# Performance work log

Hardware: AMD Instinct MI355X
Metric: run time of the kernel (lower is better)

## Reference

```python
import jax, jax.numpy as jnp
import numpy as np
from jax import lax

NH = 8          # heads
DK = 64         # total key/query depth
DV = 64         # total value depth
DKH = DK // NH  # per-head key depth = 8
DVH = DV // NH  # per-head value depth = 8
H = W = 32
CIN = 256
FILTERS = 256


def rel_to_abs(x):
    # x: [B, N, L, 2L-1] relative logits -> [B, N, L, L] absolute logits
    B, N, L, _ = x.shape
    x = jnp.pad(x, ((0, 0), (0, 0), (0, 0), (0, 1)))          # [B,N,L,2L]
    flat = x.reshape(B, N, L * 2 * L)
    flat = jnp.pad(flat, ((0, 0), (0, 0), (0, L - 1)))        # [B,N,2L^2+L-1]
    final = flat.reshape(B, N, L + 1, 2 * L - 1)
    return final[:, :, :L, L - 1:]


def rel_logits_1d(q, rel_k, h, w, perm):
    # q: [B, NH, h, w, DKH], rel_k: [2w-1, DKH]
    B = q.shape[0]
    rel = jnp.einsum('bnxyd,md->bnxym', q, rel_k)             # [B,NH,h,w,2w-1]
    rel = rel.reshape(B, NH * h, w, 2 * w - 1)
    rel = rel_to_abs(rel)                                     # [B,NH*h,w,w]
    rel = rel.reshape(B, NH, h, w, w)[:, :, :, None]          # [B,NH,h,1,w,w]
    rel = jnp.broadcast_to(rel, (B, NH, h, h, w, w))          # tile over other axis
    rel = jnp.transpose(rel, perm)
    return rel.reshape(B, NH, h * w, h * w)


def setup_inputs() -> dict:
    key = jax.random.key(0)
    ks = jax.random.split(key, 6)
    s = lambda fan_in: 1.0 / np.sqrt(fan_in)
    return {
        'x': jax.random.normal(ks[0], (8, H, W, CIN), jnp.float32),
        'conv_w': jax.random.normal(ks[1], (3, 3, CIN, FILTERS - DV), jnp.float32) * s(9 * CIN),
        'conv_b': jnp.zeros((FILTERS - DV,), jnp.float32),
        'qkv_w': jax.random.normal(ks[2], (CIN, 2 * DK + DV), jnp.float32) * s(CIN),
        'qkv_b': jnp.zeros((2 * DK + DV,), jnp.float32),
        'attn_w': jax.random.normal(ks[3], (DV, DV), jnp.float32) * s(DV),
        'attn_b': jnp.zeros((DV,), jnp.float32),
        'key_rel_w': jax.random.normal(ks[4], (2 * W - 1, DKH), jnp.float32),
        'key_rel_h': jax.random.normal(ks[5], (2 * H - 1, DKH), jnp.float32),
    }


def reference(x, conv_w, conv_b, qkv_w, qkv_b, attn_w, attn_b, key_rel_w, key_rel_h):
    B = x.shape[0]
    # standard conv branch (SAME padding)
    conv_out = lax.conv_general_dilated(
        x, conv_w, window_strides=(1, 1), padding='SAME',
        dimension_numbers=('NHWC', 'HWIO', 'NHWC')) + conv_b

    # 1x1 qkv projection
    kqv = jnp.einsum('bhwc,co->bhwo', x, qkv_w) + qkv_b
    k = kqv[..., :DK]
    q = kqv[..., DK:2 * DK] * (DKH ** -0.5)
    v = kqv[..., 2 * DK:]

    def split_heads(t, d):
        return t.reshape(B, H, W, NH, d).transpose(0, 3, 1, 2, 4)  # [B,NH,H,W,d]

    qh = split_heads(q, DKH)
    kh = split_heads(k, DKH)
    vh = split_heads(v, DVH)

    qf = qh.reshape(B, NH, H * W, DKH)
    kf = kh.reshape(B, NH, H * W, DKH)
    vf = vh.reshape(B, NH, H * W, DVH)

    logits = jnp.einsum('bnid,bnjd->bnij', qf, kf)            # [B,NH,HW,HW]
    rel_w = rel_logits_1d(qh, key_rel_w, H, W, (0, 1, 2, 4, 3, 5))
    qh_t = qh.transpose(0, 1, 3, 2, 4)                        # [B,NH,W,H,d]
    rel_h = rel_logits_1d(qh_t, key_rel_h, W, H, (0, 1, 4, 2, 5, 3))
    logits = logits + rel_w + rel_h

    weights = jax.nn.softmax(logits, axis=-1)
    attn = jnp.einsum('bnij,bnjd->bnid', weights, vf)         # [B,NH,HW,DVH]
    attn = attn.reshape(B, NH, H, W, DVH).transpose(0, 2, 3, 1, 4).reshape(B, H, W, DV)
    attn = jnp.einsum('bhwc,co->bhwo', attn, attn_w) + attn_b

    return jnp.concatenate([conv_out, attn], axis=3)
```

## Files before the change

kernel.cpp:

```cpp
#include <hip/hip_runtime.h>
#include <cstdint>

using u16 = unsigned short;
using u32 = uint32_t;

typedef __attribute__((ext_vector_type(8))) short bf16x8;
typedef __attribute__((ext_vector_type(4))) float f32x4;

__device__ __forceinline__ float bf2f(u16 v) { return __uint_as_float(((u32)v) << 16); }
__device__ __forceinline__ u16 f2bf(float f) {
    u32 u = __float_as_uint(f);
    u += 0x7fffu + ((u >> 16) & 1u);
    return (u16)(u >> 16);
}

#define FLAG_OFF 0
#define WSH_OFF  2097168
#define AWF_OFF  2588688
#define CBF_OFF  2592784
#define QBF_OFF  2592976
#define ABF_OFF  2593168
#define KRW_OFF  2593232
#define KRH_OFF  2593736
#define KB_OFF   2594240
#define QB_OFF   3118528
#define VB_OFF   3642816
#define AT_OFF   4167104
#define WSHQ_OFF 9409984

__global__ void detect_kernel(const u16* __restrict__ x, int* __restrict__ flag) {
    __shared__ int cnt;
    if (threadIdx.x == 0) cnt = 0;
    __syncthreads();
    int c = 0;
    #pragma unroll
    for (int k = 0; k < 16; k++) {
        u16 v = x[threadIdx.x * 16 + k];
        int e = (v >> 7) & 0xFF;
        c += (e >= 110 && e <= 140) ? 1 : 0;
    }
    atomicAdd(&cnt, c);
    __syncthreads();
    if (threadIdx.x == 0) *flag = (cnt > 3300) ? 1 : 0;
}

__global__ __launch_bounds__(256) void prep_kernel(
    const void* __restrict__ cw, const void* __restrict__ qw,
    const void* __restrict__ cb, const void* __restrict__ qb,
    const void* __restrict__ aw, const void* __restrict__ ab,
    const void* __restrict__ kw_, const void* __restrict__ kh_,
    u16* __restrict__ wshC, u16* __restrict__ wshQ,
    float* __restrict__ cbf, float* __restrict__ qbf, float* __restrict__ awf,
    float* __restrict__ abf, float* __restrict__ krw, float* __restrict__ krh,
    const int* __restrict__ flag)
{
    const int blk = blockIdx.x;
    const int fl = *flag;
    if (blk < 240) {
        const void* w; u16* o; int g;
        if (blk < 216) { w = cw; o = wshC; g = blk * 256 + threadIdx.x; }
        else           { w = qw; o = wshQ; g = (blk - 216) * 256 + threadIdx.x; }
        const int kk = g / 768, rem = g % 768;
        const int tile = rem >> 6, lane = rem & 63;
        const int n = tile * 16 + (lane & 15);
        u16 tmp[8];
        #pragma unroll
        for (int j = 0; j < 8; j++) {
            const size_t k = (size_t)(kk * 32 + ((lane >> 4) << 3) + j);
            tmp[j] = fl ? ((const u16*)w)[k * 192 + n]
                        : f2bf(((const float*)w)[k * 192 + n]);
        }
        *(uint4*)(o + (size_t)g * 8) = *(const uint4*)tmp;
    } else {
        const int gid = (blk - 240) * 256 + threadIdx.x;
        const void* src; float* dst; int e;
        if      (gid <  192) { src = cb;  dst = cbf; e = gid; }
        else if (gid <  384) { src = qb;  dst = qbf; e = gid - 192; }
        else if (gid < 4480) { src = aw;  dst = awf; e = gid - 384; }
        else if (gid < 4544) { src = ab;  dst = abf; e = gid - 4480; }
        else if (gid < 5048) { src = kw_; dst = krw; e = gid - 4544; }
        else if (gid < 5552) { src = kh_; dst = krh; e = gid - 5048; }
        else return;
        dst[e] = fl ? bf2f(((const u16*)src)[e]) : ((const float*)src)[e];
    }
}

__global__ __launch_bounds__(256) void qkv_mfma_kernel(
    const void* __restrict__ xr, const u16* __restrict__ wsh, const float* __restrict__ qbf_,
    const int* __restrict__ flag,
    u16* __restrict__ kb16, float* __restrict__ qbuf, u16* __restrict__ vb16)
{
    const int coh = blockIdx.x, row = blockIdx.y;
    const int b = row >> 5, h = row & 31;
    const int t = threadIdx.x;
    __shared__ u16 xs[32 * 264];
    const int fl = *flag;

    if (fl) {
        const u16* src = (const u16*)xr + (size_t)row * 8192;
        #pragma unroll
        for (int i = 0; i < 4; ++i) {
            const int idx = t + i * 256;
            const int px = idx >> 5, cq = idx & 31;
            *(uint4*)(xs + px * 264 + cq * 8) = *(const uint4*)(src + px * 256 + cq * 8);
        }
    } else {
        const float* src = (const float*)xr + (size_t)row * 8192;
        #pragma unroll
        for (int i = 0; i < 8; ++i) {
            const int idx = t + i * 256;
            const int px = idx >> 6, c4 = idx & 63;
            float4 v = *(const float4*)(src + px * 256 + c4 * 4);
            u32 lo = (u32)f2bf(v.x) | ((u32)f2bf(v.y) << 16);
            u32 hi = (u32)f2bf(v.z) | ((u32)f2bf(v.w) << 16);
            *(uint2*)(xs + px * 264 + c4 * 4) = make_uint2(lo, hi);
        }
    }
    __syncthreads();

    const int lane = t & 63, wave = t >> 6;
    const int Mtile = wave & 1;
    const int tg0 = coh * 6 + (wave >> 1) * 3;
    const int l15 = lane & 15, quad = lane >> 4;

    f32x4 acc[3] = {{0,0,0,0},{0,0,0,0},{0,0,0,0}};

    const u16* ap = xs + (Mtile * 16 + l15) * 264 + quad * 8;
    #pragma unroll
    for (int kk = 0; kk < 8; ++kk) {
        const bf16x8 av = *(const bf16x8*)(ap + kk * 32);
        const u16* wp = wsh + ((size_t)(kk * 12 + tg0) * 64 + lane) * 8;
        const bf16x8 b0 = *(const bf16x8*)(wp);
        const bf16x8 b1 = *(const bf16x8*)(wp + 512);
        const bf16x8 b2 = *(const bf16x8*)(wp + 1024);
        acc[0] = __builtin_amdgcn_mfma_f32_16x16x32_bf16(av, b0, acc[0], 0, 0, 0);
        acc[1] = __builtin_amdgcn_mfma_f32_16x16x32_bf16(av, b1, acc[1], 0, 0, 0);
        acc[2] = __builtin_amdgcn_mfma_f32_16x16x32_bf16(av, b2, acc[2], 0, 0, 0);
    }

    const int px0 = Mtile * 16 + quad * 4;
    #pragma unroll
    for (int ti = 0; ti < 3; ++ti) {
        const int tg = tg0 + ti;
        const int o = tg * 16 + l15;
        const int third = tg >> 2;
        const int within = o - third * 64;
        const int n = within >> 3, d = within & 7;
        const float bias = qbf_[o];
        #pragma unroll
        for (int r = 0; r < 4; ++r) {
            const int i = h * 32 + px0 + r;
            const size_t off = ((size_t)(b * 8 + n) * 1024 + i) * 8 + d;
            const float val = acc[ti][r] + bias;
            if (third == 0)      kb16[off] = f2bf(val);
            else if (third == 1) qbuf[off] = val * 0.51006973050f;
            else                 vb16[off] = f2bf(val);
        }
    }
}

__global__ __launch_bounds__(256) void conv_mfma_kernel(
    const void* __restrict__ xr, const u16* __restrict__ wsh, const float* __restrict__ cbf,
    const int* __restrict__ flag, void* __restrict__ out)
{
    const int coh = blockIdx.x, row = blockIdx.y;
    const int b = row >> 5, h = row & 31;
    const int t = threadIdx.x;
    __shared__ u16 xs[3 * 34 * 264];
    const int fl = *flag;

    #pragma unroll
    for (int r = 0; r < 3; ++r) {
        const int hh = h + r - 1;
        if (t < 64) {
            const int s = (t >> 5) ? 33 : 0, cq = t & 31;
            *(uint4*)(xs + (r * 34 + s) * 264 + cq * 8) = make_uint4(0, 0, 0, 0);
        }
        const bool ok = (hh >= 0) && (hh < 32);
        const size_t base = ((size_t)((b * 32 + (ok ? hh : 0)) * 32)) * 256;
        if (fl) {
            const u16* src = (const u16*)xr + base;
            #pragma unroll
            for (int i = 0; i < 4; ++i) {
                const int idx = t + i * 256;
                const int px = idx >> 5, cq = idx & 31;
                uint4 v = ok ? *(const uint4*)(src + px * 256 + cq * 8)
                             : make_uint4(0, 0, 0, 0);
                *(uint4*)(xs + (r * 34 + 1 + px) * 264 + cq * 8) = v;
            }
        } else {
            const float* src = (const float*)xr + base;
            #pragma unroll
            for (int i = 0; i < 8; ++i) {
                const int idx = t + i * 256;
                const int px = idx >> 6, c4 = idx & 63;
                float4 v = ok ? *(const float4*)(src + px * 256 + c4 * 4)
                              : make_float4(0.f, 0.f, 0.f, 0.f);
                u32 lo = (u32)f2bf(v.x) | ((u32)f2bf(v.y) << 16);
                u32 hi = (u32)f2bf(v.z) | ((u32)f2bf(v.w) << 16);
                *(uint2*)(xs + (r * 34 + 1 + px) * 264 + c4 * 4) = make_uint2(lo, hi);
            }
        }
    }
    __syncthreads();

    const int lane = t & 63, wave = t >> 6;
    const int Mtile = wave & 1;
    const int tg0 = coh * 6 + (wave >> 1) * 3;
    const int l15 = lane & 15, quad = lane >> 4;

    f32x4 acc[3] = {{0,0,0,0},{0,0,0,0},{0,0,0,0}};

    #pragma unroll
    for (int p = 0; p < 9; ++p) {
        const int kh = p / 3, kw = p - kh * 3;
        const u16* ap = xs + (kh * 34 + kw + Mtile * 16 + l15) * 264 + quad * 8;
        #pragma unroll
        for (int ck = 0; ck < 8; ++ck) {
            const int kk = p * 8 + ck;
            const bf16x8 av = *(const bf16x8*)(ap + ck * 32);
            const u16* wp = wsh + ((size_t)(kk * 12 + tg0) * 64 + lane) * 8;
            const bf16x8 b0 = *(const bf16x8*)(wp);
            const bf16x8 b1 = *(const bf16x8*)(wp + 512);
            const bf16x8 b2 = *(const bf16x8*)(wp + 1024);
            acc[0] = __builtin_amdgcn_mfma_f32_16x16x32_bf16(av, b0, acc[0], 0, 0, 0);
            acc[1] = __builtin_amdgcn_mfma_f32_16x16x32_bf16(av, b1, acc[1], 0, 0, 0);
            acc[2] = __builtin_amdgcn_mfma_f32_16x16x32_bf16(av, b2, acc[2], 0, 0, 0);
        }
    }

    const int px0 = Mtile * 16 + quad * 4;
    #pragma unroll
    for (int ti = 0; ti < 3; ++ti) {
        const int co = (tg0 + ti) * 16 + l15;
        const float bias = cbf[co];
        #pragma unroll
        for (int r = 0; r < 4; ++r) {
            const size_t oidx = ((size_t)row * 32 + px0 + r) * 256 + co;
            const float v = acc[ti][r] + bias;
            if (fl) ((u16*)out)[oidx] = f2bf(v);
            else    ((float*)out)[oidx] = v;
        }
    }
}

__global__ __launch_bounds__(256) void attn_mfma_kernel(
    const u16* __restrict__ kb16, const float* __restrict__ qbuf, const u16* __restrict__ vb16,
    const float* __restrict__ krw, const float* __restrict__ krh, float* __restrict__ attnbuf)
{
    const int qb = blockIdx.x;
    const int bn = blockIdx.y;
    const int b = bn >> 3, hn = bn & 7;
    const int t = threadIdx.x;
    const int i0 = qb * 64;

    __shared__ u16   sVT[8 * 1032];
    __shared__ u16   sRW[64 * 40];
    __shared__ float sRH[32 * 68];
    __shared__ u16   sP [4 * 16 * 56];

    const u16* vg = vb16 + (size_t)bn * 8192;
    #pragma unroll
    for (int k4 = 0; k4 < 4; k4++) {
        const int key = t + k4 * 256;
        uint4 vv = *(const uint4*)(vg + key * 8);
        sVT[0 * 1032 + key] = (u16)(vv.x);  sVT[1 * 1032 + key] = (u16)(vv.x >> 16);
        sVT[2 * 1032 + key] = (u16)(vv.y);  sVT[3 * 1032 + key] = (u16)(vv.y >> 16);
        sVT[4 * 1032 + key] = (u16)(vv.z);  sVT[5 * 1032 + key] = (u16)(vv.z >> 16);
        sVT[6 * 1032 + key] = (u16)(vv.w);  sVT[7 * 1032 + key] = (u16)(vv.w >> 16);
    }
    #pragma unroll
    for (int k8 = 0; k8 < 8; k8++) {
        const int idx = t + k8 * 256;
        const int il = idx >> 5, w = idx & 31;
        const int i = i0 + il;
        const float* q = qbuf + ((size_t)bn * 1024 + i) * 8;
        float4 qa = *(const float4*)q, qc = *(const float4*)(q + 4);
        const float* rp = krw + (size_t)(w - (i & 31) + 31) * 8;
        float4 ra = *(const float4*)rp, rc = *(const float4*)(rp + 4);
        sRW[il * 40 + w] = f2bf(qa.x*ra.x + qa.y*ra.y + qa.z*ra.z + qa.w*ra.w
                              + qc.x*rc.x + qc.y*rc.y + qc.z*rc.z + qc.w*rc.w);
        const float* hp = krh + (size_t)(w - (i >> 5) + 31) * 8;
        float4 ha = *(const float4*)hp, hc = *(const float4*)(hp + 4);
        sRH[w * 68 + il] = qa.x*ha.x + qa.y*ha.y + qa.z*ha.z + qa.w*ha.w
                         + qc.x*hc.x + qc.y*hc.y + qc.z*hc.z + qc.w*hc.w;
    }
    __syncthreads();

    const int lane = t & 63, wave = t >> 6;
    const int l15 = lane & 15, quad = lane >> 4;

    union Frag { u16 a[8]; bf16x8 v; };
    Frag Aq;
    {
        const float* q = qbuf + ((size_t)bn * 1024 + i0 + wave * 16 + l15) * 8;
        float4 qa = *(const float4*)q, qc = *(const float4*)(q + 4);
        Aq.a[0] = f2bf(qa.x); Aq.a[1] = f2bf(qa.y); Aq.a[2] = f2bf(qa.z); Aq.a[3] = f2bf(qa.w);
        Aq.a[4] = f2bf(qc.x); Aq.a[5] = f2bf(qc.y); Aq.a[6] = f2bf(qc.z); Aq.a[7] = f2bf(qc.w);
        if (quad != 0) {
            #pragma unroll
            for (int j = 0; j < 8; j++) Aq.a[j] = 0;
        }
    }
    const bf16x8 Arw = *(const bf16x8*)(sRW + (wave * 16 + l15) * 40 + quad * 8);

    Frag P0, P1, ONE;
    #pragma unroll
    for (int j = 0; j < 8; j++) { P0.a[j] = 0; P1.a[j] = 0; ONE.a[j] = 0x3F80; }
    {
        const int h0 = l15 - quad * 8;
        if (h0 >= 0 && h0 < 8) P0.a[h0] = 0x3F80;
        const int h1 = 16 + l15 - quad * 8;
        if (h1 >= 0 && h1 < 8) P1.a[h1] = 0x3F80;
    }

    const u16* kg = kb16 + (size_t)bn * 8192;
    u16* pb = sP + wave * (16 * 56);
    f32x4 oacc = {0.f, 0.f, 0.f, 0.f};

    for (int chunk = 0; chunk < 32; chunk++) {
        const float4 rh4 = *(const float4*)(sRH + chunk * 68 + wave * 16 + quad * 4);
        f32x4 acc0 = {rh4.x, rh4.y, rh4.z, rh4.w};
        f32x4 acc1 = acc0;
        const bf16x8 bk0 = *(const bf16x8*)(kg + (chunk * 32 + l15) * 8);
        const bf16x8 bk1 = *(const bf16x8*)(kg + (chunk * 32 + 16 + l15) * 8);
        acc0 = __builtin_amdgcn_mfma_f32_16x16x32_bf16(Aq.v, bk0, acc0, 0, 0, 0);
        acc0 = __builtin_amdgcn_mfma_f32_16x16x32_bf16(Arw, P0.v, acc0, 0, 0, 0);
        acc1 = __builtin_amdgcn_mfma_f32_16x16x32_bf16(Aq.v, bk1, acc1, 0, 0, 0);
        acc1 = __builtin_amdgcn_mfma_f32_16x16x32_bf16(Arw, P1.v, acc1, 0, 0, 0);
        #pragma unroll
        for (int r = 0; r < 4; r++) {
            const float p0 = exp2f(fminf(acc0[r], 80.0f));
            const float p1 = exp2f(fminf(acc1[r], 80.0f));
            pb[(quad * 4 + r) * 56 + l15]      = f2bf(p0);
            pb[(quad * 4 + r) * 56 + 16 + l15] = f2bf(p1);
        }
        const bf16x8 Ap = *(const bf16x8*)(pb + l15 * 56 + quad * 8);
        bf16x8 Bv;
        if (l15 < 8) Bv = *(const bf16x8*)(sVT + l15 * 1032 + chunk * 32 + quad * 8);
        else         Bv = ONE.v;
        oacc = __builtin_amdgcn_mfma_f32_16x16x32_bf16(Ap, Bv, oacc, 0, 0, 0);
    }

    #pragma unroll
    for (int r = 0; r < 4; r++) {
        const float lr = __shfl(oacc[r], (lane & 48) | 8, 64);
        const float val = oacc[r] / fmaxf(lr, 1e-30f);
        if (l15 < 8) {
            const int i = i0 + wave * 16 + quad * 4 + r;
            attnbuf[((size_t)b * 1024 + i) * 64 + hn * 8 + l15] = val;
        }
    }
}

__global__ __launch_bounds__(256) void proj_kernel(
    const float* __restrict__ attnbuf, const float* __restrict__ awf, const float* __restrict__ abf,
    const int* __restrict__ flag, void* __restrict__ out)
{
    const int g = blockIdx.x * 256 + threadIdx.x;
    const int px = g >> 6, o = g & 63;
    const float* ar = attnbuf + (size_t)px * 64;
    float acc = abf[o];
    #pragma unroll 8
    for (int c = 0; c < 64; c++) acc += ar[c] * awf[c * 64 + o];
    if (*flag) ((u16*)out)[(size_t)px * 256 + 192 + o] = f2bf(acc);
    else       ((float*)out)[(size_t)px * 256 + 192 + o] = acc;
}

extern "C" void kernel_launch(void* const* d_in, const int* in_sizes, int n_in,
                              void* d_out, int out_size, void* d_ws, size_t ws_size,
                              hipStream_t stream)
{
    float* ws = (float*)d_ws;
    int*   flag = (int*)(ws + FLAG_OFF);
    u16*   wsh  = (u16*)(ws + WSH_OFF);
    float* awf  = ws + AWF_OFF;
    float* cbf  = ws + CBF_OFF;
    float* qbf  = ws + QBF_OFF;
    float* abf  = ws + ABF_OFF;
    float* krw  = ws + KRW_OFF;
    float* krh  = ws + KRH_OFF;
    u16*   kb16 = (u16*)(ws + KB_OFF);
    float* qbuf = ws + QB_OFF;
    u16*   vb16 = (u16*)(ws + VB_OFF);
    float* atb  = ws + AT_OFF;
    u16*   wshQ = (u16*)(ws + WSHQ_OFF);

    detect_kernel<<<1, 256, 0, stream>>>((const u16*)d_in[0], flag);

    prep_kernel<<<262, 256, 0, stream>>>(
        d_in[1], d_in[3], d_in[2], d_in[4], d_in[5], d_in[6], d_in[7], d_in[8],
        wsh, wshQ, cbf, qbf, awf, abf, krw, krh, flag);

    qkv_mfma_kernel <<<dim3(2, 256), 256, 0, stream>>>(d_in[0], wshQ, qbf, flag, kb16, qbuf, vb16);
    conv_mfma_kernel<<<dim3(2, 256), 256, 0, stream>>>(d_in[0], wsh, cbf, flag, d_out);
    attn_mfma_kernel<<<dim3(16, 64), 256, 0, stream>>>(kb16, qbuf, vb16, krw, krh, atb);
    proj_kernel     <<<2048,         256, 0, stream>>>(atb, awf, abf, flag, d_out);
}
```

Baseline: 173.5 us.

## Split attention keys across wave pairs and store V pre-transposed in global

The qkv kernel now writes V directly in a transposed [d][key] layout, so the attention kernel reads V fragments from global memory instead of staging a transposed copy in shared memory. Each attention block now handles 32 queries instead of 64, and two waves split the 32 key chunks per 16-query tile, then merge partial outputs and denominators through shared memory before normalising. This doubles the grid and shortens the serial key loop, at the cost of an extra barrier, a shared-memory merge, and recomputing the relative-logit tables per smaller block. The exp clamp to 80 is removed, which drops a safety guard against overflow.

```diff
diff --git a/kernel.cpp b/kernel.cpp
--- a/kernel.cpp
+++ b/kernel.cpp
@@ -88,7 +88,7 @@
 __global__ __launch_bounds__(256) void qkv_mfma_kernel(
     const void* __restrict__ xr, const u16* __restrict__ wsh, const float* __restrict__ qbf_,
     const int* __restrict__ flag,
-    u16* __restrict__ kb16, float* __restrict__ qbuf, u16* __restrict__ vb16)
+    u16* __restrict__ kb16, float* __restrict__ qbuf, u16* __restrict__ vt16)
 {
     const int coh = blockIdx.x, row = blockIdx.y;
     const int b = row >> 5, h = row & 31;
@@ -150,11 +150,13 @@
         #pragma unroll
         for (int r = 0; r < 4; ++r) {
             const int i = h * 32 + px0 + r;
-            const size_t off = ((size_t)(b * 8 + n) * 1024 + i) * 8 + d;
             const float val = acc[ti][r] + bias;
-            if (third == 0)      kb16[off] = f2bf(val);
-            else if (third == 1) qbuf[off] = val * 0.51006973050f;
-            else                 vb16[off] = f2bf(val);
+            if (third == 0)
+                kb16[((size_t)(b * 8 + n) * 1024 + i) * 8 + d] = f2bf(val);
+            else if (third == 1)
+                qbuf[((size_t)(b * 8 + n) * 1024 + i) * 8 + d] = val * 0.51006973050f;
+            else
+                vt16[((size_t)(b * 8 + n) * 8 + d) * 1024 + i] = f2bf(val);
         }
     }
 }
@@ -245,33 +247,23 @@
 }
 
 __global__ __launch_bounds__(256) void attn_mfma_kernel(
-    const u16* __restrict__ kb16, const float* __restrict__ qbuf, const u16* __restrict__ vb16,
+    const u16* __restrict__ kb16, const float* __restrict__ qbuf, const u16* __restrict__ vt16,
     const float* __restrict__ krw, const float* __restrict__ krh, float* __restrict__ attnbuf)
 {
     const int qb = blockIdx.x;
     const int bn = blockIdx.y;
     const int b = bn >> 3, hn = bn & 7;
     const int t = threadIdx.x;
-    const int i0 = qb * 64;
-
-    __shared__ u16   sVT[8 * 1032];
-    __shared__ u16   sRW[64 * 40];
-    __shared__ float sRH[32 * 68];
+    const int i0 = qb * 32;
+
+    __shared__ u16   sRW[32 * 40];
+    __shared__ float sRH[32 * 36];
     __shared__ u16   sP [4 * 16 * 56];
-
-    const u16* vg = vb16 + (size_t)bn * 8192;
+    __shared__ float sMG[2 * 16 * 17];
+
     #pragma unroll
     for (int k4 = 0; k4 < 4; k4++) {
-        const int key = t + k4 * 256;
-        uint4 vv = *(const uint4*)(vg + key * 8);
-        sVT[0 * 1032 + key] = (u16)(vv.x);  sVT[1 * 1032 + key] = (u16)(vv.x >> 16);
-        sVT[2 * 1032 + key] = (u16)(vv.y);  sVT[3 * 1032 + key] = (u16)(vv.y >> 16);
-        sVT[4 * 1032 + key] = (u16)(vv.z);  sVT[5 * 1032 + key] = (u16)(vv.z >> 16);
-        sVT[6 * 1032 + key] = (u16)(vv.w);  sVT[7 * 1032 + key] = (u16)(vv.w >> 16);
-    }
-    #pragma unroll
-    for (int k8 = 0; k8 < 8; k8++) {
-        const int idx = t + k8 * 256;
+        const int idx = t + k4 * 256;
         const int il = idx >> 5, w = idx & 31;
         const int i = i0 + il;
         const float* q = qbuf + ((size_t)bn * 1024 + i) * 8;
@@ -282,18 +274,20 @@
                               + qc.x*rc.x + qc.y*rc.y + qc.z*rc.z + qc.w*rc.w);
         const float* hp = krh + (size_t)(w - (i >> 5) + 31) * 8;
         float4 ha = *(const float4*)hp, hc = *(const float4*)(hp + 4);
-        sRH[w * 68 + il] = qa.x*ha.x + qa.y*ha.y + qa.z*ha.z + qa.w*ha.w
+        sRH[w * 36 + il] = qa.x*ha.x + qa.y*ha.y + qa.z*ha.z + qa.w*ha.w
                          + qc.x*hc.x + qc.y*hc.y + qc.z*hc.z + qc.w*hc.w;
     }
     __syncthreads();
 
     const int lane = t & 63, wave = t >> 6;
     const int l15 = lane & 15, quad = lane >> 4;
+    const int Mtile = wave >> 1;
+    const int ch0 = (wave & 1) * 16;
 
     union Frag { u16 a[8]; bf16x8 v; };
     Frag Aq;
     {
-        const float* q = qbuf + ((size_t)bn * 1024 + i0 + wave * 16 + l15) * 8;
+        const float* q = qbuf + ((size_t)bn * 1024 + i0 + Mtile * 16 + l15) * 8;
         float4 qa = *(const float4*)q, qc = *(const float4*)(q + 4);
         Aq.a[0] = f2bf(qa.x); Aq.a[1] = f2bf(qa.y); Aq.a[2] = f2bf(qa.z); Aq.a[3] = f2bf(qa.w);
         Aq.a[4] = f2bf(qc.x); Aq.a[5] = f2bf(qc.y); Aq.a[6] = f2bf(qc.z); Aq.a[7] = f2bf(qc.w);
@@ -302,7 +296,7 @@
             for (int j = 0; j < 8; j++) Aq.a[j] = 0;
         }
     }
-    const bf16x8 Arw = *(const bf16x8*)(sRW + (wave * 16 + l15) * 40 + quad * 8);
+    const bf16x8 Arw = *(const bf16x8*)(sRW + (Mtile * 16 + l15) * 40 + quad * 8);
 
     Frag P0, P1, ONE;
     #pragma unroll
@@ -315,11 +309,13 @@
     }
 
     const u16* kg = kb16 + (size_t)bn * 8192;
+    const u16* vt = vt16 + (size_t)bn * 8192;
     u16* pb = sP + wave * (16 * 56);
     f32x4 oacc = {0.f, 0.f, 0.f, 0.f};
 
-    for (int chunk = 0; chunk < 32; chunk++) {
-        const float4 rh4 = *(const float4*)(sRH + chunk * 68 + wave * 16 + quad * 4);
+    for (int c = 0; c < 16; c++) {
+        const int chunk = ch0 + c;
+        const float4 rh4 = *(const float4*)(sRH + chunk * 36 + Mtile * 16 + quad * 4);
         f32x4 acc0 = {rh4.x, rh4.y, rh4.z, rh4.w};
         f32x4 acc1 = acc0;
         const bf16x8 bk0 = *(const bf16x8*)(kg + (chunk * 32 + l15) * 8);
@@ -330,25 +326,34 @@
         acc1 = __builtin_amdgcn_mfma_f32_16x16x32_bf16(Arw, P1.v, acc1, 0, 0, 0);
         #pragma unroll
         for (int r = 0; r < 4; r++) {
-            const float p0 = exp2f(fminf(acc0[r], 80.0f));
-            const float p1 = exp2f(fminf(acc1[r], 80.0f));
+            const float p0 = exp2f(acc0[r]);
+            const float p1 = exp2f(acc1[r]);
             pb[(quad * 4 + r) * 56 + l15]      = f2bf(p0);
             pb[(quad * 4 + r) * 56 + 16 + l15] = f2bf(p1);
         }
         const bf16x8 Ap = *(const bf16x8*)(pb + l15 * 56 + quad * 8);
         bf16x8 Bv;
-        if (l15 < 8) Bv = *(const bf16x8*)(sVT + l15 * 1032 + chunk * 32 + quad * 8);
+        if (l15 < 8) Bv = *(const bf16x8*)(vt + l15 * 1024 + chunk * 32 + quad * 8);
         else         Bv = ONE.v;
         oacc = __builtin_amdgcn_mfma_f32_16x16x32_bf16(Ap, Bv, oacc, 0, 0, 0);
     }
 
-    #pragma unroll
-    for (int r = 0; r < 4; r++) {
-        const float lr = __shfl(oacc[r], (lane & 48) | 8, 64);
-        const float val = oacc[r] / fmaxf(lr, 1e-30f);
-        if (l15 < 8) {
-            const int i = i0 + wave * 16 + quad * 4 + r;
-            attnbuf[((size_t)b * 1024 + i) * 64 + hn * 8 + l15] = val;
+    if (wave & 1) {
+        #pragma unroll
+        for (int r = 0; r < 4; r++)
+            sMG[(Mtile * 16 + quad * 4 + r) * 17 + l15] = oacc[r];
+    }
+    __syncthreads();
+    if (!(wave & 1)) {
+        #pragma unroll
+        for (int r = 0; r < 4; r++) {
+            oacc[r] += sMG[(Mtile * 16 + quad * 4 + r) * 17 + l15];
+            const float lr = __shfl(oacc[r], (lane & 48) | 8, 64);
+            const float val = oacc[r] / fmaxf(lr, 1e-30f);
+            if (l15 < 8) {
+                const int i = i0 + Mtile * 16 + quad * 4 + r;
+                attnbuf[((size_t)b * 1024 + i) * 64 + hn * 8 + l15] = val;
+            }
         }
     }
 }
@@ -382,7 +387,7 @@
     float* krh  = ws + KRH_OFF;
     u16*   kb16 = (u16*)(ws + KB_OFF);
     float* qbuf = ws + QB_OFF;
-    u16*   vb16 = (u16*)(ws + VB_OFF);
+    u16*   vt16 = (u16*)(ws + VB_OFF);
     float* atb  = ws + AT_OFF;
     u16*   wshQ = (u16*)(ws + WSHQ_OFF);
 
@@ -392,8 +397,8 @@
         d_in[1], d_in[3], d_in[2], d_in[4], d_in[5], d_in[6], d_in[7], d_in[8],
         wsh, wshQ, cbf, qbf, awf, abf, krw, krh, flag);
 
-    qkv_mfma_kernel <<<dim3(2, 256), 256, 0, stream>>>(d_in[0], wshQ, qbf, flag, kb16, qbuf, vb16);
+    qkv_mfma_kernel <<<dim3(2, 256), 256, 0, stream>>>(d_in[0], wshQ, qbf, flag, kb16, qbuf, vt16);
     conv_mfma_kernel<<<dim3(2, 256), 256, 0, stream>>>(d_in[0], wsh, cbf, flag, d_out);
-    attn_mfma_kernel<<<dim3(16, 64), 256, 0, stream>>>(kb16, qbuf, vb16, krw, krh, atb);
+    attn_mfma_kernel<<<dim3(32, 64), 256, 0, stream>>>(kb16, qbuf, vt16, krw, krh, atb);
     proj_kernel     <<<2048,         256, 0, stream>>>(atb, awf, abf, flag, d_out);
 }
```

Result: no change. 174.8 us (+0.7%).
